# Performance work log

Measured on AMD Instinct MI355X. Metric: run time of the kernel, lower is better.

The kernel has to match this reference:

```python
import jax, jax.numpy as jnp
import numpy as np

B, S, H, E, K = 2, 1024, 1024, 8, 2
F = 4 * H


def setup_inputs() -> dict:
    key = jax.random.key(0)
    ks = jax.random.split(key, 8)
    std = 0.02
    return {
        "x": jax.random.normal(ks[0], (B, S, H), jnp.float32),
        "gate_w": jax.random.normal(ks[1], (E, H), jnp.float32) * (std / np.sqrt(H)),
        "gate_bias": jnp.zeros((E,), jnp.float32),
        "Wu": jax.random.normal(ks[2], (E, F, H), jnp.float32) * std,
        "bu": jnp.zeros((E, F), jnp.float32),
        "Wd": jax.random.normal(ks[3], (E, H, F), jnp.float32) * std,
        "bd": jnp.zeros((E, H), jnp.float32),
        "sWu": jax.random.normal(ks[4], (F, H), jnp.float32) * std,
        "sbu": jnp.zeros((F,), jnp.float32),
        "sWd": jax.random.normal(ks[5], (H, F), jnp.float32) * std,
        "sbd": jnp.zeros((H,), jnp.float32),
    }


def reference(x, gate_w, gate_bias, Wu, bu, Wd, bd, sWu, sbu, sWd, sbd):
    b, s, h = x.shape
    x_flat = x.reshape(-1, h)                      # [T, H]
    T = x_flat.shape[0]
    # Sigmoid gating + top-k (bias added before sigmoid, as in source)
    scores = jax.nn.sigmoid(x_flat @ gate_w.T + gate_bias)          # [T, E]
    top_scores, top_idx = jax.lax.top_k(scores, K)                  # [T, K]
    top_scores = top_scores / (top_scores.sum(-1, keepdims=True) + 1e-6)
    # Per-token per-expert combine weights (0 for non-selected experts)
    w = jnp.zeros((T, E), x.dtype).at[jnp.arange(T)[:, None], top_idx].add(top_scores)
    # Dense per-expert FFN over all tokens; masked out by w where not routed.
    h1 = jnp.einsum('th,efh->etf', x_flat, Wu) + bu[:, None, :]     # [E, T, F]
    a1 = jax.nn.gelu(h1, approximate=False)
    y = jnp.einsum('etf,ehf->eth', a1, Wd) + bd[:, None, :]         # [E, T, H]
    combined = jnp.einsum('te,eth->th', w, y)                       # [T, H]
    # Shared expert, scaled by 0.1
    sh = jax.nn.gelu(x_flat @ sWu.T + sbu, approximate=False)
    shared = (sh @ sWd.T + sbd) * 0.1
    return (combined + shared).reshape(b, s, h)
```

## Files before the change

kernel.cpp:

```cpp
#include <hip/hip_runtime.h>
#include <cstdint>
#include <cstddef>

#define T_TOK 2048
#define H_DIM 1024
#define E_NUM 8
#define F_DIM 4096
#define NG 9

typedef unsigned short ushort_t;
typedef __attribute__((ext_vector_type(8))) short bf16x8;
typedef __attribute__((ext_vector_type(4))) float f32x4;
typedef unsigned int u32;
typedef u32 __attribute__((address_space(3))) lds_u32;
typedef u32 __attribute__((address_space(1))) glob_u32;

constexpr size_t OFF_TTI = 0;
constexpr size_t OFF_TTW = 16u << 10;
constexpr size_t OFF_CNT = 32u << 10;
constexpr size_t OFF_OFFS = (32u << 10) + 256;
constexpr size_t OFF_RID = 64u << 10;
constexpr size_t OFF_WTS = 96u << 10;
constexpr size_t OFF_XBF = 1u << 20;
constexpr size_t OFF_WUB = 8u << 20;
constexpr size_t OFF_WDB = 80u << 20;
constexpr size_t OFF_A   = 152u << 20;

__device__ __forceinline__ ushort_t f2bf(float f) {
  union { float f; unsigned u; } v; v.f = f;
  unsigned r = v.u + 0x7FFFu + ((v.u >> 16) & 1u);
  return (ushort_t)(r >> 16);
}

__device__ __forceinline__ float gelu_exact(float v) {
  return 0.5f * v * (1.0f + erff(v * 0.70710678118654752f));
}

__device__ __forceinline__ void gll16(const ushort_t* g, ushort_t* l) {
  __builtin_amdgcn_global_load_lds((glob_u32*)(g), (lds_u32*)(l), 16, 0, 0);
}

__global__ __launch_bounds__(256) void route_k(const float* __restrict__ x,
                                               const float* __restrict__ gw,
                                               const float* __restrict__ gb,
                                               int* __restrict__ tt_idx,
                                               float* __restrict__ tt_w) {
  const int lane = threadIdx.x & 63;
  const int wid = threadIdx.x >> 6;
  const int t = blockIdx.x * 4 + wid;
  if (t >= T_TOK) return;
  const float* xr = x + (size_t)t * H_DIM;
  float acc[8] = {0.f, 0.f, 0.f, 0.f, 0.f, 0.f, 0.f, 0.f};
  for (int i = 0; i < H_DIM; i += 64) {
    const int k = i + lane;
    const float xv = xr[k];
#pragma unroll
    for (int e = 0; e < 8; ++e) acc[e] = fmaf(xv, gw[e * H_DIM + k], acc[e]);
  }
#pragma unroll
  for (int e = 0; e < 8; ++e) {
    float v = acc[e];
#pragma unroll
    for (int s = 32; s; s >>= 1) v += __shfl_xor(v, s, 64);
    acc[e] = v;
  }
  if (lane == 0) {
    float sc[8];
#pragma unroll
    for (int e = 0; e < 8; ++e) sc[e] = 1.0f / (1.0f + expf(-(acc[e] + gb[e])));
    int i0 = 0;
#pragma unroll
    for (int e = 1; e < 8; ++e) if (sc[e] > sc[i0]) i0 = e;
    int i1 = (i0 == 0) ? 1 : 0;
#pragma unroll
    for (int e = 0; e < 8; ++e) if (e != i0 && sc[e] > sc[i1]) i1 = e;
    const float d = sc[i0] + sc[i1] + 1e-6f;
    tt_idx[2 * t] = i0;
    tt_idx[2 * t + 1] = i1;
    tt_w[2 * t] = sc[i0] / d;
    tt_w[2 * t + 1] = sc[i1] / d;
  }
}

__global__ __launch_bounds__(256) void build_k(const int* __restrict__ tt_idx,
                                               const float* __restrict__ tt_w,
                                               int* __restrict__ counts,
                                               int* __restrict__ offs,
                                               int* __restrict__ rid,
                                               float* __restrict__ wts) {
  __shared__ int cnt[NG];
  __shared__ int cur[NG];
  const int tid = threadIdx.x;
  if (tid < NG) cnt[tid] = 0;
  __syncthreads();
  for (int p = tid; p < 2 * T_TOK; p += 256) atomicAdd(&cnt[tt_idx[p]], 1);
  __syncthreads();
  if (tid == 0) {
    int run = 0;
    for (int e = 0; e < E_NUM; ++e) {
      offs[e] = run;
      counts[e] = cnt[e];
      cur[e] = run;
      run += cnt[e];
    }
    offs[E_NUM] = 2 * T_TOK;
    counts[E_NUM] = T_TOK;
    cur[E_NUM] = 2 * T_TOK;
  }
  __syncthreads();
  for (int p = tid; p < 2 * T_TOK; p += 256) {
    const int e = tt_idx[p];
    const int pos = atomicAdd(&cur[e], 1);
    rid[pos] = ((p >> 1) << 2) | (p & 1);
    wts[pos] = tt_w[p];
  }
  for (int p = tid; p < T_TOK; p += 256) {
    rid[2 * T_TOK + p] = (p << 2) | 2;
    wts[2 * T_TOK + p] = 0.1f;
  }
}

__global__ __launch_bounds__(256) void convert_k(const float* __restrict__ Wu,
                                                 const float* __restrict__ sWu,
                                                 const float* __restrict__ Wd,
                                                 const float* __restrict__ sWd,
                                                 const float* __restrict__ x,
                                                 ushort_t* __restrict__ Wub,
                                                 ushort_t* __restrict__ Wdb,
                                                 ushort_t* __restrict__ Xbf) {
  const long WE = (long)NG * F_DIM * H_DIM;
  const long W8 = (long)8 * F_DIM * H_DIM;
  const long XE = (long)T_TOK * H_DIM;
  const long total = (2 * WE + XE) / 8;
  for (long i = blockIdx.x * 256L + threadIdx.x; i < total; i += (long)gridDim.x * 256L) {
    const long base = i * 8;
    const float* src;
    ushort_t* dst;
    if (base < WE) {
      const long o = base;
      src = (o < W8) ? (Wu + o) : (sWu + (o - W8));
      dst = Wub + o;
    } else if (base < 2 * WE) {
      const long o = base - WE;
      src = (o < W8) ? (Wd + o) : (sWd + (o - W8));
      dst = Wdb + o;
    } else {
      const long o = base - 2 * WE;
      src = x + o;
      dst = Xbf + o;
    }
    const float4 v0 = *(const float4*)src;
    const float4 v1 = *(const float4*)(src + 4);
    bf16x8 r;
    r[0] = (short)f2bf(v0.x); r[1] = (short)f2bf(v0.y);
    r[2] = (short)f2bf(v0.z); r[3] = (short)f2bf(v0.w);
    r[4] = (short)f2bf(v1.x); r[5] = (short)f2bf(v1.y);
    r[6] = (short)f2bf(v1.z); r[7] = (short)f2bf(v1.w);
    *(bf16x8*)dst = r;
  }
}

__global__ __launch_bounds__(256) void bias_init(const int* __restrict__ tt_idx,
                                                 const float* __restrict__ tt_w,
                                                 const float* __restrict__ bd,
                                                 const float* __restrict__ sbd,
                                                 float* __restrict__ out) {
  const int t = blockIdx.x;
  const int h = threadIdx.x * 4;
  const int e0 = tt_idx[2 * t];
  const int e1 = tt_idx[2 * t + 1];
  const float w0 = tt_w[2 * t];
  const float w1 = tt_w[2 * t + 1];
  const float4 b0 = *(const float4*)(bd + (size_t)e0 * H_DIM + h);
  const float4 b1 = *(const float4*)(bd + (size_t)e1 * H_DIM + h);
  const float4 bs = *(const float4*)(sbd + h);
  float4 o;
  o.x = w0 * b0.x + w1 * b1.x + 0.1f * bs.x;
  o.y = w0 * b0.y + w1 * b1.y + 0.1f * bs.y;
  o.z = w0 * b0.z + w1 * b1.z + 0.1f * bs.z;
  o.w = w0 * b0.w + w1 * b1.w + 0.1f * bs.w;
  *(float4*)(out + (size_t)t * H_DIM + h) = o;
}

__global__ __launch_bounds__(256) void up_gemm(const ushort_t* __restrict__ Xbf,
                                               const ushort_t* __restrict__ Wub,
                                               const int* __restrict__ counts,
                                               const int* __restrict__ offs,
                                               const int* __restrict__ rid,
                                               const float* __restrict__ wts,
                                               const float* __restrict__ bu,
                                               const float* __restrict__ sbu,
                                               ushort_t* __restrict__ Aout) {
  const int g = blockIdx.y >> 4;
  const int mt = blockIdx.y & 15;
  const int rows = counts[g];
  if (mt * 128 >= rows) return;
  const int off = offs[g];
  const int n0 = blockIdx.x * 128;

  __shared__ ushort_t lA[128 * 64];
  __shared__ ushort_t lB[128 * 64];

  const int tid = threadIdx.x;
  const int lane = tid & 63;
  const int wid = tid >> 6;
  const int sr = lane >> 3;
  const int swz = ((lane & 7) ^ sr) << 3;

  const ushort_t* Wg = Wub + (size_t)g * F_DIM * H_DIM;
  const ushort_t* pA[4];
  const ushort_t* pB[4];
#pragma unroll
  for (int i = 0; i < 4; ++i) {
    const int rA = (wid * 4 + i) * 8 + sr;
    int ig = mt * 128 + rA;
    if (ig >= rows) ig = rows - 1;
    pA[i] = Xbf + (size_t)(rid[off + ig] >> 2) * H_DIM + swz;
    pB[i] = Wg + (size_t)(n0 + rA) * H_DIM + swz;
  }

  f32x4 acc[4][4];
#pragma unroll
  for (int m = 0; m < 4; ++m)
#pragma unroll
    for (int n = 0; n < 4; ++n) acc[m][n] = (f32x4){0.f, 0.f, 0.f, 0.f};

  const int wr = (wid >> 1) * 64;
  const int wc = (wid & 1) * 64;
  const int fr = lane & 15;
  const int hi = lane >> 4;

  for (int k0 = 0; k0 < H_DIM; k0 += 64) {
    __syncthreads();
#pragma unroll
    for (int i = 0; i < 4; ++i) {
      gll16(pA[i] + k0, &lA[(wid * 4 + i) * 512]);
      gll16(pB[i] + k0, &lB[(wid * 4 + i) * 512]);
    }
    __syncthreads();
#pragma unroll
    for (int ks = 0; ks < 2; ++ks) {
      const int cc = ks * 4 + hi;
      bf16x8 af[4], bv[4];
#pragma unroll
      for (int m = 0; m < 4; ++m) {
        const int r = wr + m * 16 + fr;
        af[m] = *(const bf16x8*)&lA[r * 64 + ((cc ^ (r & 7)) << 3)];
      }
#pragma unroll
      for (int n = 0; n < 4; ++n) {
        const int r = wc + n * 16 + fr;
        bv[n] = *(const bf16x8*)&lB[r * 64 + ((cc ^ (r & 7)) << 3)];
      }
#pragma unroll
      for (int m = 0; m < 4; ++m)
#pragma unroll
        for (int n = 0; n < 4; ++n)
          acc[m][n] = __builtin_amdgcn_mfma_f32_16x16x32_bf16(af[m], bv[n], acc[m][n], 0, 0, 0);
    }
  }

  const float* bug = (g < E_NUM) ? (bu + (size_t)g * F_DIM) : sbu;
#pragma unroll
  for (int m = 0; m < 4; ++m) {
#pragma unroll
    for (int q = 0; q < 4; ++q) {
      const int r = wr + m * 16 + hi * 4 + q;
      const int ig = mt * 128 + r;
      if (ig < rows) {
        const float wrow = wts[off + ig];
        const size_t rowbase = (size_t)(off + ig) * F_DIM + n0;
#pragma unroll
        for (int n = 0; n < 4; ++n) {
          const int c = wc + n * 16 + fr;
          const float v = acc[m][n][q] + bug[n0 + c];
          Aout[rowbase + c] = f2bf(gelu_exact(v) * wrow);
        }
      }
    }
  }
}

__global__ __launch_bounds__(256) void down_gemm(const ushort_t* __restrict__ Ain,
                                                 const ushort_t* __restrict__ Wdb,
                                                 const int* __restrict__ counts,
                                                 const int* __restrict__ offs,
                                                 const int* __restrict__ rid,
                                                 float* __restrict__ out) {
  const int g = blockIdx.y >> 4;
  const int mt = blockIdx.y & 15;
  const int rows = counts[g];
  if (mt * 128 >= rows) return;
  const int off = offs[g];
  const int n0 = blockIdx.x * 128;
  const int kbase = blockIdx.z * 1024;

  __shared__ ushort_t lA[128 * 64];
  __shared__ ushort_t lB[128 * 64];

  const int tid = threadIdx.x;
  const int lane = tid & 63;
  const int wid = tid >> 6;
  const int sr = lane >> 3;
  const int swz = ((lane & 7) ^ sr) << 3;

  const ushort_t* Wg = Wdb + (size_t)g * H_DIM * F_DIM;
  const ushort_t* pA[4];
  const ushort_t* pB[4];
#pragma unroll
  for (int i = 0; i < 4; ++i) {
    const int rA = (wid * 4 + i) * 8 + sr;
    pA[i] = Ain + (size_t)(off + mt * 128 + rA) * F_DIM + kbase + swz;
    pB[i] = Wg + (size_t)(n0 + rA) * F_DIM + kbase + swz;
  }

  f32x4 acc[4][4];
#pragma unroll
  for (int m = 0; m < 4; ++m)
#pragma unroll
    for (int n = 0; n < 4; ++n) acc[m][n] = (f32x4){0.f, 0.f, 0.f, 0.f};

  const int wr = (wid >> 1) * 64;
  const int wc = (wid & 1) * 64;
  const int fr = lane & 15;
  const int hi = lane >> 4;

  for (int k0 = 0; k0 < 1024; k0 += 64) {
    __syncthreads();
#pragma unroll
    for (int i = 0; i < 4; ++i) {
      gll16(pA[i] + k0, &lA[(wid * 4 + i) * 512]);
      gll16(pB[i] + k0, &lB[(wid * 4 + i) * 512]);
    }
    __syncthreads();
#pragma unroll
    for (int ks = 0; ks < 2; ++ks) {
      const int cc = ks * 4 + hi;
      bf16x8 af[4], bv[4];
#pragma unroll
      for (int m = 0; m < 4; ++m) {
        const int r = wr + m * 16 + fr;
        af[m] = *(const bf16x8*)&lA[r * 64 + ((cc ^ (r & 7)) << 3)];
      }
#pragma unroll
      for (int n = 0; n < 4; ++n) {
        const int r = wc + n * 16 + fr;
        bv[n] = *(const bf16x8*)&lB[r * 64 + ((cc ^ (r & 7)) << 3)];
      }
#pragma unroll
      for (int m = 0; m < 4; ++m)
#pragma unroll
        for (int n = 0; n < 4; ++n)
          acc[m][n] = __builtin_amdgcn_mfma_f32_16x16x32_bf16(af[m], bv[n], acc[m][n], 0, 0, 0);
    }
  }

#pragma unroll
  for (int m = 0; m < 4; ++m) {
#pragma unroll
    for (int q = 0; q < 4; ++q) {
      const int r = wr + m * 16 + hi * 4 + q;
      const int ig = mt * 128 + r;
      if (ig < rows) {
        const int rv = rid[off + ig];
        float* orow = out + (size_t)(rv >> 2) * H_DIM + n0;
#pragma unroll
        for (int n = 0; n < 4; ++n) {
          const int c = wc + n * 16 + fr;
          unsafeAtomicAdd(&orow[c], acc[m][n][q]);
        }
      }
    }
  }
}

extern "C" void kernel_launch(void* const* d_in, const int* in_sizes, int n_in,
                              void* d_out, int out_size, void* d_ws, size_t ws_size,
                              hipStream_t stream) {
  (void)in_sizes; (void)n_in; (void)out_size; (void)ws_size;
  const float* x = (const float*)d_in[0];
  const float* gate_w = (const float*)d_in[1];
  const float* gate_b = (const float*)d_in[2];
  const float* Wu = (const float*)d_in[3];
  const float* bu = (const float*)d_in[4];
  const float* Wd = (const float*)d_in[5];
  const float* bd = (const float*)d_in[6];
  const float* sWu = (const float*)d_in[7];
  const float* sbu = (const float*)d_in[8];
  const float* sWd = (const float*)d_in[9];
  const float* sbd = (const float*)d_in[10];
  float* out = (float*)d_out;

  char* ws = (char*)d_ws;
  int* tt_idx = (int*)(ws + OFF_TTI);
  float* tt_w = (float*)(ws + OFF_TTW);
  int* counts = (int*)(ws + OFF_CNT);
  int* offs = (int*)(ws + OFF_OFFS);
  int* rid = (int*)(ws + OFF_RID);
  float* wts = (float*)(ws + OFF_WTS);
  ushort_t* Xbf = (ushort_t*)(ws + OFF_XBF);
  ushort_t* Wub = (ushort_t*)(ws + OFF_WUB);
  ushort_t* Wdb = (ushort_t*)(ws + OFF_WDB);
  ushort_t* A = (ushort_t*)(ws + OFF_A);

  hipLaunchKernelGGL(route_k, dim3(T_TOK / 4), dim3(256), 0, stream,
                     x, gate_w, gate_b, tt_idx, tt_w);
  hipLaunchKernelGGL(build_k, dim3(1), dim3(256), 0, stream,
                     tt_idx, tt_w, counts, offs, rid, wts);
  hipLaunchKernelGGL(bias_init, dim3(T_TOK), dim3(256), 0, stream,
                     tt_idx, tt_w, bd, sbd, out);
  hipLaunchKernelGGL(convert_k, dim3(4096), dim3(256), 0, stream,
                     Wu, sWu, Wd, sWd, x, Wub, Wdb, Xbf);
  hipLaunchKernelGGL(up_gemm, dim3(F_DIM / 128, NG * 16), dim3(256), 0, stream,
                     Xbf, Wub, counts, offs, rid, wts, bu, sbu, A);
  hipLaunchKernelGGL(down_gemm, dim3(H_DIM / 128, NG * 16, 4), dim3(256), 0, stream,
                     A, Wdb, counts, offs, rid, out);
}
```

Before: 633.6 us.

## Replace down-GEMM atomic scatter with bf16 partial buffers and a combine kernel

The down GEMM no longer atomically adds fp32 results into the output. It writes bf16 partials into a per-token, per-slot buffer (two routed slots plus the shared expert), with the split-K reduced from 4 to 2. A new combine kernel sums the partials and adds the weighted biases, which replaces the bias_init kernel. This removes atomic contention and the extra output initialization pass. In exchange it adds an extra kernel, extra global traffic, and bf16 rounding of the partial sums. Halving the z-dimension also gives each block twice as many K iterations, so there are fewer blocks to parallelize across.

Measured after the change: 593.6 us. 1.07x faster.

```diff
diff --git a/kernel.cpp b/kernel.cpp
--- a/kernel.cpp
+++ b/kernel.cpp
@@ -25,11 +25,18 @@
 constexpr size_t OFF_WUB = 8u << 20;
 constexpr size_t OFF_WDB = 80u << 20;
 constexpr size_t OFF_A   = 152u << 20;
+constexpr size_t OFF_Y   = 200u << 20;
+constexpr size_t Y_SPLIT_STRIDE = (size_t)T_TOK * 3 * H_DIM;
 
 __device__ __forceinline__ ushort_t f2bf(float f) {
   union { float f; unsigned u; } v; v.f = f;
   unsigned r = v.u + 0x7FFFu + ((v.u >> 16) & 1u);
   return (ushort_t)(r >> 16);
+}
+
+__device__ __forceinline__ float bf2f(ushort_t b) {
+  union { unsigned u; float f; } v; v.u = ((unsigned)b) << 16;
+  return v.f;
 }
 
 __device__ __forceinline__ float gelu_exact(float v) {
@@ -160,28 +167,6 @@
   }
 }
 
-__global__ __launch_bounds__(256) void bias_init(const int* __restrict__ tt_idx,
-                                                 const float* __restrict__ tt_w,
-                                                 const float* __restrict__ bd,
-                                                 const float* __restrict__ sbd,
-                                                 float* __restrict__ out) {
-  const int t = blockIdx.x;
-  const int h = threadIdx.x * 4;
-  const int e0 = tt_idx[2 * t];
-  const int e1 = tt_idx[2 * t + 1];
-  const float w0 = tt_w[2 * t];
-  const float w1 = tt_w[2 * t + 1];
-  const float4 b0 = *(const float4*)(bd + (size_t)e0 * H_DIM + h);
-  const float4 b1 = *(const float4*)(bd + (size_t)e1 * H_DIM + h);
-  const float4 bs = *(const float4*)(sbd + h);
-  float4 o;
-  o.x = w0 * b0.x + w1 * b1.x + 0.1f * bs.x;
-  o.y = w0 * b0.y + w1 * b1.y + 0.1f * bs.y;
-  o.z = w0 * b0.z + w1 * b1.z + 0.1f * bs.z;
-  o.w = w0 * b0.w + w1 * b1.w + 0.1f * bs.w;
-  *(float4*)(out + (size_t)t * H_DIM + h) = o;
-}
-
 __global__ __launch_bounds__(256) void up_gemm(const ushort_t* __restrict__ Xbf,
                                                const ushort_t* __restrict__ Wub,
                                                const int* __restrict__ counts,
@@ -286,14 +271,15 @@
                                                  const int* __restrict__ counts,
                                                  const int* __restrict__ offs,
                                                  const int* __restrict__ rid,
-                                                 float* __restrict__ out) {
+                                                 ushort_t* __restrict__ Ybf) {
   const int g = blockIdx.y >> 4;
   const int mt = blockIdx.y & 15;
   const int rows = counts[g];
   if (mt * 128 >= rows) return;
   const int off = offs[g];
   const int n0 = blockIdx.x * 128;
-  const int kbase = blockIdx.z * 1024;
+  const int kbase = blockIdx.z * 2048;
+  ushort_t* Ys = Ybf + (size_t)blockIdx.z * Y_SPLIT_STRIDE;
 
   __shared__ ushort_t lA[128 * 64];
   __shared__ ushort_t lB[128 * 64];
@@ -325,7 +311,7 @@
   const int fr = lane & 15;
   const int hi = lane >> 4;
 
-  for (int k0 = 0; k0 < 1024; k0 += 64) {
+  for (int k0 = 0; k0 < 2048; k0 += 64) {
     __syncthreads();
 #pragma unroll
     for (int i = 0; i < 4; ++i) {
@@ -363,15 +349,48 @@
       const int ig = mt * 128 + r;
       if (ig < rows) {
         const int rv = rid[off + ig];
-        float* orow = out + (size_t)(rv >> 2) * H_DIM + n0;
+        ushort_t* yrow = Ys + ((size_t)(rv >> 2) * 3 + (rv & 3)) * H_DIM + n0;
 #pragma unroll
         for (int n = 0; n < 4; ++n) {
           const int c = wc + n * 16 + fr;
-          unsafeAtomicAdd(&orow[c], acc[m][n][q]);
+          yrow[c] = f2bf(acc[m][n][q]);
         }
       }
     }
   }
+}
+
+__global__ __launch_bounds__(256) void combine_k(const ushort_t* __restrict__ Ybf,
+                                                 const int* __restrict__ tt_idx,
+                                                 const float* __restrict__ tt_w,
+                                                 const float* __restrict__ bd,
+                                                 const float* __restrict__ sbd,
+                                                 float* __restrict__ out) {
+  const int t = blockIdx.x;
+  const int h = threadIdx.x * 4;
+  const int e0 = tt_idx[2 * t];
+  const int e1 = tt_idx[2 * t + 1];
+  const float w0 = tt_w[2 * t];
+  const float w1 = tt_w[2 * t + 1];
+  float s[4] = {0.f, 0.f, 0.f, 0.f};
+#pragma unroll
+  for (int sp = 0; sp < 2; ++sp) {
+#pragma unroll
+    for (int sl = 0; sl < 3; ++sl) {
+      const ushort_t* yp = Ybf + sp * Y_SPLIT_STRIDE + ((size_t)t * 3 + sl) * H_DIM + h;
+      const ushort4 v = *(const ushort4*)yp;
+      s[0] += bf2f(v.x); s[1] += bf2f(v.y); s[2] += bf2f(v.z); s[3] += bf2f(v.w);
+    }
+  }
+  const float4 b0 = *(const float4*)(bd + (size_t)e0 * H_DIM + h);
+  const float4 b1 = *(const float4*)(bd + (size_t)e1 * H_DIM + h);
+  const float4 bs = *(const float4*)(sbd + h);
+  float4 o;
+  o.x = s[0] + w0 * b0.x + w1 * b1.x + 0.1f * bs.x;
+  o.y = s[1] + w0 * b0.y + w1 * b1.y + 0.1f * bs.y;
+  o.z = s[2] + w0 * b0.z + w1 * b1.z + 0.1f * bs.z;
+  o.w = s[3] + w0 * b0.w + w1 * b1.w + 0.1f * bs.w;
+  *(float4*)(out + (size_t)t * H_DIM + h) = o;
 }
 
 extern "C" void kernel_launch(void* const* d_in, const int* in_sizes, int n_in,
@@ -402,17 +421,18 @@
   ushort_t* Wub = (ushort_t*)(ws + OFF_WUB);
   ushort_t* Wdb = (ushort_t*)(ws + OFF_WDB);
   ushort_t* A = (ushort_t*)(ws + OFF_A);
+  ushort_t* Y = (ushort_t*)(ws + OFF_Y);
 
   hipLaunchKernelGGL(route_k, dim3(T_TOK / 4), dim3(256), 0, stream,
                      x, gate_w, gate_b, tt_idx, tt_w);
   hipLaunchKernelGGL(build_k, dim3(1), dim3(256), 0, stream,
                      tt_idx, tt_w, counts, offs, rid, wts);
-  hipLaunchKernelGGL(bias_init, dim3(T_TOK), dim3(256), 0, stream,
-                     tt_idx, tt_w, bd, sbd, out);
   hipLaunchKernelGGL(convert_k, dim3(4096), dim3(256), 0, stream,
                      Wu, sWu, Wd, sWd, x, Wub, Wdb, Xbf);
   hipLaunchKernelGGL(up_gemm, dim3(F_DIM / 128, NG * 16), dim3(256), 0, stream,
                      Xbf, Wub, counts, offs, rid, wts, bu, sbu, A);
-  hipLaunchKernelGGL(down_gemm, dim3(H_DIM / 128, NG * 16, 4), dim3(256), 0, stream,
-                     A, Wdb, counts, offs, rid, out);
-}
+  hipLaunchKernelGGL(down_gemm, dim3(H_DIM / 128, NG * 16, 2), dim3(256), 0, stream,
+                     A, Wdb, counts, offs, rid, Y);
+  hipLaunchKernelGGL(combine_k, dim3(T_TOK), dim3(256), 0, stream,
+                     Y, tt_idx, tt_w, bd, sbd, out);
+}
```
